# Kernel tuning notes

Hardware: AMD Instinct MI355X
Metric: run time of the kernel (lower is better)

The kernel has to match this reference:

```python
import jax, jax.numpy as jnp
import numpy as np

R = 2            # radius
KS = 2 * R + 1   # kernel size = 5
K2 = KS * KS     # 25 neighbors per pixel
TOPK = 10
TAU = 0.1
EPS = 1e-8


def _unfold(x):
    """x: [B,C,H,W] -> patches [B,C,K2,H,W], zero-padded like F.unfold(padding=R)."""
    B, C, H, W = x.shape
    xp = jnp.pad(x, ((0, 0), (0, 0), (R, R), (R, R)))
    shifts = [xp[:, :, dy:dy + H, dx:dx + W] for dy in range(KS) for dx in range(KS)]
    return jnp.stack(shifts, axis=2)


def setup_inputs() -> dict:
    key = jax.random.key(0)
    kx, = jax.random.split(key, 1)
    x = jax.random.normal(kx, (4, 256, 56, 56), dtype=jnp.float32)
    gamma = jnp.asarray(0.2, dtype=jnp.float32)  # nn.Parameter scalar, init lam=0.2
    return {"x": x, "gamma": gamma}


def reference(x, gamma):
    xd = jax.lax.stop_gradient(x)  # detach_target=True
    patches = _unfold(xd)                         # [B,C,K2,H,W]
    center = xd[:, :, None]                       # [B,C,1,H,W]
    # cosine similarity over channel dim, scaled by 1/tau
    dot = jnp.sum(patches * center, axis=1)       # [B,K2,H,W]
    pn = jnp.sqrt(jnp.sum(patches * patches, axis=1))
    cn = jnp.sqrt(jnp.sum(center * center, axis=1))
    sims = dot / jnp.maximum(pn * cn, EPS) / TAU  # [B,K2,H,W]
    # top-k mask along neighbor dim, then softmax over kept entries
    s = jnp.moveaxis(sims, 1, -1)                 # [B,H,W,K2]
    _, idx = jax.lax.top_k(s, TOPK)               # idx: [B,H,W,TOPK]
    keep = jnp.sum(jax.nn.one_hot(idx, K2, dtype=jnp.float32), axis=-2) > 0  # [B,H,W,K2]
    masked = jnp.where(keep, s, -jnp.inf)
    w = jax.nn.softmax(masked, axis=-1)           # [B,H,W,K2]
    w = jnp.moveaxis(w, -1, 1)                    # [B,K2,H,W]
    y = jnp.einsum('bckhw,bkhw->bchw', patches, w)
    return x + gamma * y
```

## Files before the change

kernel.cpp:

```cpp
#include <hip/hip_runtime.h>
#include <hip/hip_bf16.h>


#define PX 3136
#define CS 3136

typedef float f4a __attribute__((ext_vector_type(4), aligned(4)));

#define DECODE_SLAB()                                   \
    const int bid   = blockIdx.x;                       \
    const int xcd   = bid & 7;                          \
    const int b     = xcd >> 1;                         \
    const int pbase = (((xcd & 1) * 49) + (bid >> 3)) * 32;

__global__ __launch_bounds__(1024) void k_dot(const float* __restrict__ x,
                                              float* __restrict__ dot) {
    DECODE_SLAB();
    const int px = threadIdx.x & 31;
    const int ck = threadIdx.x >> 5;
    const int p  = pbase + px;
    const int h  = p / 56;
    const int w  = p - h * 56;

    const bool vm2 = (h >= 2), vm1 = (h >= 1);
    const bool cv0 = (w >= 2), cv1 = (w >= 1), cv3 = (w <= 54), cv4 = (w <= 53);

    const float* xb  = x + (size_t)b * 256 * CS + (size_t)ck * 8 * CS;
    const float* cp  = xb + p;
    const float* pr2 = cp - 112;
    const float* pr1 = cp - 56;

    float a[13];
    #pragma unroll
    for (int i = 0; i < 13; ++i) a[i] = 0.f;

    {
        const float ctr = cp[0];
        float n;
        n = (vm2 && cv0) ? pr2[-2] : 0.f; a[0]  = fmaf(ctr, n, a[0]);
        n = (vm2 && cv1) ? pr2[-1] : 0.f; a[1]  = fmaf(ctr, n, a[1]);
        n =  vm2         ? pr2[ 0] : 0.f; a[2]  = fmaf(ctr, n, a[2]);
        n = (vm2 && cv3) ? pr2[ 1] : 0.f; a[3]  = fmaf(ctr, n, a[3]);
        n = (vm2 && cv4) ? pr2[ 2] : 0.f; a[4]  = fmaf(ctr, n, a[4]);
        n = (vm1 && cv0) ? pr1[-2] : 0.f; a[5]  = fmaf(ctr, n, a[5]);
        n = (vm1 && cv1) ? pr1[-1] : 0.f; a[6]  = fmaf(ctr, n, a[6]);
        n =  vm1         ? pr1[ 0] : 0.f; a[7]  = fmaf(ctr, n, a[7]);
        n = (vm1 && cv3) ? pr1[ 1] : 0.f; a[8]  = fmaf(ctr, n, a[8]);
        n = (vm1 && cv4) ? pr1[ 2] : 0.f; a[9]  = fmaf(ctr, n, a[9]);
        n =  cv0         ? cp [-2] : 0.f; a[10] = fmaf(ctr, n, a[10]);
        n =  cv1         ? cp [-1] : 0.f; a[11] = fmaf(ctr, n, a[11]);
        a[12] = fmaf(ctr, ctr, a[12]);
    }

    const bool tail_unsafe = (b == 3) && (ck == 31);

    #pragma unroll
    for (int c = 1; c < 8; ++c) {
        const int o = c * CS;
        if (c == 7 && tail_unsafe) {
            const f4a   t2  = *(const f4a*)(pr2 + o - 2);
            const float t2e = pr2[o + 2];
            const f4a   t1  = *(const f4a*)(pr1 + o - 2);
            const float t1e = pr1[o + 2];
            const float c0  = cp[o - 2], c1 = cp[o - 1], ctr = cp[o];
            a[0]  = fmaf(ctr, t2.x, a[0]);
            a[1]  = fmaf(ctr, t2.y, a[1]);
            a[2]  = fmaf(ctr, t2.z, a[2]);
            a[3]  = fmaf(ctr, t2.w, a[3]);
            a[4]  = fmaf(ctr, t2e,  a[4]);
            a[5]  = fmaf(ctr, t1.x, a[5]);
            a[6]  = fmaf(ctr, t1.y, a[6]);
            a[7]  = fmaf(ctr, t1.z, a[7]);
            a[8]  = fmaf(ctr, t1.w, a[8]);
            a[9]  = fmaf(ctr, t1e,  a[9]);
            a[10] = fmaf(ctr, c0,   a[10]);
            a[11] = fmaf(ctr, c1,   a[11]);
            a[12] = fmaf(ctr, ctr,  a[12]);
        } else {
            const f4a   t2  = *(const f4a*)(pr2 + o - 2);
            const float t2e = pr2[o + 2];
            const f4a   t1  = *(const f4a*)(pr1 + o - 2);
            const float t1e = pr1[o + 2];
            const f4a   t0  = *(const f4a*)(cp  + o - 2);
            const float ctr = t0.z;
            a[0]  = fmaf(ctr, t2.x, a[0]);
            a[1]  = fmaf(ctr, t2.y, a[1]);
            a[2]  = fmaf(ctr, t2.z, a[2]);
            a[3]  = fmaf(ctr, t2.w, a[3]);
            a[4]  = fmaf(ctr, t2e,  a[4]);
            a[5]  = fmaf(ctr, t1.x, a[5]);
            a[6]  = fmaf(ctr, t1.y, a[6]);
            a[7]  = fmaf(ctr, t1.z, a[7]);
            a[8]  = fmaf(ctr, t1.w, a[8]);
            a[9]  = fmaf(ctr, t1e,  a[9]);
            a[10] = fmaf(ctr, t0.x, a[10]);
            a[11] = fmaf(ctr, t0.y, a[11]);
            a[12] = fmaf(ctr, ctr,  a[12]);
        }
    }

    __shared__ float part[32][13][32];
    #pragma unroll
    for (int i = 0; i < 13; ++i) part[ck][i][px] = a[i];
    __syncthreads();

    if (threadIdx.x < 13 * 32) {
        const int acc = threadIdx.x >> 5, pp = threadIdx.x & 31;
        float s = 0.f;
        #pragma unroll
        for (int j = 0; j < 32; ++j) s += part[j][acc][pp];
        dot[((size_t)(b * 13 + acc)) * PX + pbase + pp] = s;
    }
}

__global__ __launch_bounds__(1024) void k_fused(const float* __restrict__ x,
                                                const float* __restrict__ dot,
                                                const float* __restrict__ gptr,
                                                float* __restrict__ out) {
    DECODE_SLAB();
    const int tid = threadIdx.x;
    const float* db = dot + (size_t)b * 13 * PX;

    __shared__ float s_lds[32][25];
    __shared__ float e_lds[32][25];
    __shared__ float inv_lds[32];

    if (tid < 800) {
        const int px = tid / 25, k = tid - (tid / 25) * 25;
        const int p = pbase + px;
        const int h = p / 56, w = p - (p / 56) * 56;
        const int dy = k / 5 - 2, dx = k % 5 - 2;
        const int rr = h + dy, cc = w + dx;
        const bool v = (rr >= 0) && (rr < 56) && (cc >= 0) && (cc < 56);
        float d = 0.f, n2 = 0.f;
        if (v) {
            const int q = rr * 56 + cc;
            n2 = db[12 * PX + q];
            d  = (k <= 12) ? db[k * PX + p] : db[(24 - k) * PX + q];
        }
        const float cn = sqrtf(db[12 * PX + p]);
        s_lds[px][k] = d / fmaxf(sqrtf(n2) * cn, 1e-8f) * 10.f;
    }
    __syncthreads();

    if (tid < 800) {
        const int px = tid / 25, k = tid - (tid / 25) * 25;
        const float sk = s_lds[px][k];
        int rank = 0;
        float m = sk;
        #pragma unroll
        for (int j = 0; j < 25; ++j) {
            const float sj = s_lds[px][j];
            rank += (int)((sj > sk) || ((sj == sk) && (j < k)));
            m = fmaxf(m, sj);
        }
        e_lds[px][k] = (rank < 10) ? __expf(sk - m) : 0.f;
    }
    __syncthreads();

    if (tid < 32) {
        float denom = 0.f;
        #pragma unroll
        for (int k = 0; k < 25; ++k) denom += e_lds[tid][k];
        inv_lds[tid] = 1.f / denom;
    }
    __syncthreads();

    const int px  = tid & 31;
    const int sub = tid >> 5;
    const int p   = pbase + px;
    const int h   = p / 56;
    const int w   = p - h * 56;
    const float g = *gptr;

    const bool vm2 = (h >= 2), vm1 = (h >= 1), vp1 = (h <= 54), vp2 = (h <= 53);
    const bool cv0 = (w >= 2), cv1 = (w >= 1), cv3 = (w <= 54), cv4 = (w <= 53);

    const float inv = inv_lds[px];
    float wq[25];
    #pragma unroll
    for (int k = 0; k < 25; ++k) {
        const int dy = k / 5 - 2, dx = k % 5 - 2;
        const bool vr = (dy == -2) ? vm2 : (dy == -1) ? vm1 : (dy == 0) ? true
                      : (dy == 1) ? vp1 : vp2;
        const bool vc = (dx == -2) ? cv0 : (dx == -1) ? cv1 : (dx == 0) ? true
                      : (dx == 1) ? cv3 : cv4;
        wq[k] = (vr && vc) ? e_lds[px][k] * inv : 0.f;
    }

    const float* xb = x   + ((size_t)b * 256 + sub * 8) * CS;
    float*       ob = out + ((size_t)b * 256 + sub * 8) * CS;

    #pragma unroll 2
    for (int ci = 0; ci < 8; ++ci) {
        const float* xp = xb + ci * CS + p;
        const bool unsafe = (b == 0 && sub == 0 && ci == 0) ||
                            (b == 3 && sub == 31 && ci == 7);
        float y = 0.f, ctr;
        if (!unsafe) {
            #pragma unroll
            for (int r = 0; r < 5; ++r) {
                const float* rp = xp + (r - 2) * 56;
                const f4a   v4 = *(const f4a*)(rp - 2);
                const float s4 = rp[2];
                if (r == 2) ctr = v4.z;
                y = fmaf(wq[r*5+0], v4.x, y);
                y = fmaf(wq[r*5+1], v4.y, y);
                y = fmaf(wq[r*5+2], v4.z, y);
                y = fmaf(wq[r*5+3], v4.w, y);
                y = fmaf(wq[r*5+4], s4,   y);
            }
        } else {
            ctr = xp[0];
            #pragma unroll
            for (int k = 0; k < 25; ++k) {
                const int dy = k / 5 - 2, dx = k % 5 - 2;
                const bool vr = (dy == -2) ? vm2 : (dy == -1) ? vm1 : (dy == 0) ? true
                              : (dy == 1) ? vp1 : vp2;
                const bool vc = (dx == -2) ? cv0 : (dx == -1) ? cv1 : (dx == 0) ? true
                              : (dx == 1) ? cv3 : cv4;
                const float xv = (vr && vc) ? xp[dy * 56 + dx] : 0.f;
                y = fmaf(wq[k], xv, y);
            }
        }
        ob[ci * CS + p] = ctr + g * y;
    }
}

extern "C" void kernel_launch(void* const* d_in, const int* in_sizes, int n_in,
                              void* d_out, int out_size, void* d_ws, size_t ws_size,
                              hipStream_t stream) {
    const float* x     = (const float*)d_in[0];
    const float* gamma = (const float*)d_in[1];
    float* out = (float*)d_out;
    float* dot = (float*)d_ws;

    k_dot<<<392, 1024, 0, stream>>>(x, dot);
    k_fused<<<392, 1024, 0, stream>>>(x, dot, gamma, out);
}
```

Measured before the change: 32.53 us.

## Map k_fused blocks to image rows and share neighbors via wave shuffles

The fused kernel now gives each block one full image row (56 pixels, 224 blocks) instead of 32-pixel slabs. Each lane of a 64-wide wave owns one column and loads five row values per channel. Horizontal neighbors come from cross-lane shuffles instead of overlapping unaligned vector loads, and edge handling uses clamped row offsets plus zeroed weights. This drops the special 'unsafe' path and the redundant loads, but leaves 8 of 64 lanes idle, runs fewer blocks, and gives each wave 16 channels.

After: 36.57 us. +12.4%, slower.

```diff
diff --git a/kernel.cpp b/kernel.cpp
--- a/kernel.cpp
+++ b/kernel.cpp
@@ -117,20 +117,22 @@
                                                 const float* __restrict__ dot,
                                                 const float* __restrict__ gptr,
                                                 float* __restrict__ out) {
-    DECODE_SLAB();
+    const int bid = blockIdx.x;
+    const int xcd = bid & 7;
+    const int b   = xcd >> 1;
+    const int h   = (xcd & 1) * 28 + (bid >> 3);
     const int tid = threadIdx.x;
     const float* db = dot + (size_t)b * 13 * PX;
 
-    __shared__ float s_lds[32][25];
-    __shared__ float e_lds[32][25];
-    __shared__ float inv_lds[32];
-
-    if (tid < 800) {
-        const int px = tid / 25, k = tid - (tid / 25) * 25;
-        const int p = pbase + px;
-        const int h = p / 56, w = p - (p / 56) * 56;
+    __shared__ float s_lds[56][25];
+    __shared__ float e_lds[56][25];
+    __shared__ float inv_lds[56];
+
+    for (int i = tid; i < 1400; i += 1024) {
+        const int px = i / 25, k = i - px * 25;
+        const int p = h * 56 + px;
         const int dy = k / 5 - 2, dx = k % 5 - 2;
-        const int rr = h + dy, cc = w + dx;
+        const int rr = h + dy, cc = px + dx;
         const bool v = (rr >= 0) && (rr < 56) && (cc >= 0) && (cc < 56);
         float d = 0.f, n2 = 0.f;
         if (v) {
@@ -143,8 +145,8 @@
     }
     __syncthreads();
 
-    if (tid < 800) {
-        const int px = tid / 25, k = tid - (tid / 25) * 25;
+    for (int i = tid; i < 1400; i += 1024) {
+        const int px = i / 25, k = i - px * 25;
         const float sk = s_lds[px][k];
         int rank = 0;
         float m = sk;
@@ -158,7 +160,7 @@
     }
     __syncthreads();
 
-    if (tid < 32) {
+    if (tid < 56) {
         float denom = 0.f;
         #pragma unroll
         for (int k = 0; k < 25; ++k) denom += e_lds[tid][k];
@@ -166,65 +168,55 @@
     }
     __syncthreads();
 
-    const int px  = tid & 31;
-    const int sub = tid >> 5;
-    const int p   = pbase + px;
-    const int h   = p / 56;
-    const int w   = p - h * 56;
-    const float g = *gptr;
-
-    const bool vm2 = (h >= 2), vm1 = (h >= 1), vp1 = (h <= 54), vp2 = (h <= 53);
-    const bool cv0 = (w >= 2), cv1 = (w >= 1), cv3 = (w <= 54), cv4 = (w <= 53);
-
-    const float inv = inv_lds[px];
+    const int lane = tid & 63;
+    const int wave = tid >> 6;
+    const int wc   = (lane < 56) ? lane : 55;
+    const float g  = *gptr;
+
+    const float inv = inv_lds[wc];
     float wq[25];
     #pragma unroll
     for (int k = 0; k < 25; ++k) {
         const int dy = k / 5 - 2, dx = k % 5 - 2;
-        const bool vr = (dy == -2) ? vm2 : (dy == -1) ? vm1 : (dy == 0) ? true
-                      : (dy == 1) ? vp1 : vp2;
-        const bool vc = (dx == -2) ? cv0 : (dx == -1) ? cv1 : (dx == 0) ? true
-                      : (dx == 1) ? cv3 : cv4;
-        wq[k] = (vr && vc) ? e_lds[px][k] * inv : 0.f;
-    }
-
-    const float* xb = x   + ((size_t)b * 256 + sub * 8) * CS;
-    float*       ob = out + ((size_t)b * 256 + sub * 8) * CS;
+        const int rr = h + dy, cc = lane + dx;
+        const bool v = (rr >= 0) && (rr < 56) && (cc >= 0) && (cc < 56) &&
+                       (lane < 56);
+        wq[k] = v ? e_lds[wc][k] * inv : 0.f;
+    }
+
+    const int rm2 = ((h >= 2) ? h - 2 : 0) * 56;
+    const int rm1 = ((h >= 1) ? h - 1 : 0) * 56;
+    const int r0  = h * 56;
+    const int rp1 = ((h <= 54) ? h + 1 : 55) * 56;
+    const int rp2 = ((h <= 53) ? h + 2 : 55) * 56;
+
+    const float* xb = x   + ((size_t)b * 256 + wave * 16) * CS;
+    float*       ob = out + ((size_t)b * 256 + wave * 16) * CS;
+
+#define ROW5(vr, base)                                         \
+    y = fmaf(wq[(base)+0], __shfl((vr), lane - 2, 64), y);     \
+    y = fmaf(wq[(base)+1], __shfl((vr), lane - 1, 64), y);     \
+    y = fmaf(wq[(base)+2], (vr), y);                           \
+    y = fmaf(wq[(base)+3], __shfl((vr), lane + 1, 64), y);     \
+    y = fmaf(wq[(base)+4], __shfl((vr), lane + 2, 64), y);
 
     #pragma unroll 2
-    for (int ci = 0; ci < 8; ++ci) {
-        const float* xp = xb + ci * CS + p;
-        const bool unsafe = (b == 0 && sub == 0 && ci == 0) ||
-                            (b == 3 && sub == 31 && ci == 7);
-        float y = 0.f, ctr;
-        if (!unsafe) {
-            #pragma unroll
-            for (int r = 0; r < 5; ++r) {
-                const float* rp = xp + (r - 2) * 56;
-                const f4a   v4 = *(const f4a*)(rp - 2);
-                const float s4 = rp[2];
-                if (r == 2) ctr = v4.z;
-                y = fmaf(wq[r*5+0], v4.x, y);
-                y = fmaf(wq[r*5+1], v4.y, y);
-                y = fmaf(wq[r*5+2], v4.z, y);
-                y = fmaf(wq[r*5+3], v4.w, y);
-                y = fmaf(wq[r*5+4], s4,   y);
-            }
-        } else {
-            ctr = xp[0];
-            #pragma unroll
-            for (int k = 0; k < 25; ++k) {
-                const int dy = k / 5 - 2, dx = k % 5 - 2;
-                const bool vr = (dy == -2) ? vm2 : (dy == -1) ? vm1 : (dy == 0) ? true
-                              : (dy == 1) ? vp1 : vp2;
-                const bool vc = (dx == -2) ? cv0 : (dx == -1) ? cv1 : (dx == 0) ? true
-                              : (dx == 1) ? cv3 : cv4;
-                const float xv = (vr && vc) ? xp[dy * 56 + dx] : 0.f;
-                y = fmaf(wq[k], xv, y);
-            }
-        }
-        ob[ci * CS + p] = ctr + g * y;
-    }
+    for (int ci = 0; ci < 16; ++ci) {
+        const float* xc = xb + ci * CS;
+        const float v0 = xc[rm2 + wc];
+        const float v1 = xc[rm1 + wc];
+        const float v2 = xc[r0  + wc];
+        const float v3 = xc[rp1 + wc];
+        const float v4 = xc[rp2 + wc];
+        float y = 0.f;
+        ROW5(v0, 0)
+        ROW5(v1, 5)
+        ROW5(v2, 10)
+        ROW5(v3, 15)
+        ROW5(v4, 20)
+        if (lane < 56) ob[ci * CS + r0 + lane] = v2 + g * y;
+    }
+#undef ROW5
 }
 
 extern "C" void kernel_launch(void* const* d_in, const int* in_sizes, int n_in,
@@ -236,5 +228,5 @@
     float* dot = (float*)d_ws;
 
     k_dot<<<392, 1024, 0, stream>>>(x, dot);
-    k_fused<<<392, 1024, 0, stream>>>(x, dot, gamma, out);
+    k_fused<<<224, 1024, 0, stream>>>(x, dot, gamma, out);
 }
```

## Stage input row tiles in LDS for the weighted neighbor aggregation

Applied to the files above, without the earlier changes.

The aggregation phase no longer reads 5x5 neighborhoods straight from global memory. It now loops over 8 groups of 32 channels, cooperatively copying the six needed image rows per channel into shared memory (clamped at the image borders), and computes the weighted sum from LDS. Each thread now owns one channel per group instead of eight consecutive channels. The aim is to drop redundant global and L1 neighborhood loads and the special-case path for unsafe boundary reads. In exchange it adds two block-wide barriers per group, serializes the load and compute phases, and uses about 43KB of LDS. Column-boundary taps can read uninitialized padding words, which are only cancelled by zero weights.

Measured after the change: 38.46 us. 1.18x slower.

```diff
diff --git a/kernel.cpp b/kernel.cpp
--- a/kernel.cpp
+++ b/kernel.cpp
@@ -121,6 +121,7 @@
     const int tid = threadIdx.x;
     const float* db = dot + (size_t)b * 13 * PX;
 
+    __shared__ float dlds[32 * 336 + 8];
     __shared__ float s_lds[32][25];
     __shared__ float e_lds[32][25];
     __shared__ float inv_lds[32];
@@ -173,6 +174,10 @@
     const int w   = p - h * 56;
     const float g = *gptr;
 
+    const int r0    = pbase / 56;
+    const int rbase = r0 - 2;
+    const int lrow  = h - rbase;
+
     const bool vm2 = (h >= 2), vm1 = (h >= 1), vp1 = (h <= 54), vp2 = (h <= 53);
     const bool cv0 = (w >= 2), cv1 = (w >= 1), cv3 = (w <= 54), cv4 = (w <= 53);
 
@@ -188,42 +193,42 @@
         wq[k] = (vr && vc) ? e_lds[px][k] * inv : 0.f;
     }
 
-    const float* xb = x   + ((size_t)b * 256 + sub * 8) * CS;
-    float*       ob = out + ((size_t)b * 256 + sub * 8) * CS;
-
-    #pragma unroll 2
-    for (int ci = 0; ci < 8; ++ci) {
-        const float* xp = xb + ci * CS + p;
-        const bool unsafe = (b == 0 && sub == 0 && ci == 0) ||
-                            (b == 3 && sub == 31 && ci == 7);
-        float y = 0.f, ctr;
-        if (!unsafe) {
-            #pragma unroll
-            for (int r = 0; r < 5; ++r) {
-                const float* rp = xp + (r - 2) * 56;
-                const f4a   v4 = *(const f4a*)(rp - 2);
-                const float s4 = rp[2];
-                if (r == 2) ctr = v4.z;
-                y = fmaf(wq[r*5+0], v4.x, y);
-                y = fmaf(wq[r*5+1], v4.y, y);
-                y = fmaf(wq[r*5+2], v4.z, y);
-                y = fmaf(wq[r*5+3], v4.w, y);
-                y = fmaf(wq[r*5+4], s4,   y);
-            }
-        } else {
-            ctr = xp[0];
-            #pragma unroll
-            for (int k = 0; k < 25; ++k) {
-                const int dy = k / 5 - 2, dx = k % 5 - 2;
-                const bool vr = (dy == -2) ? vm2 : (dy == -1) ? vm1 : (dy == 0) ? true
-                              : (dy == 1) ? vp1 : vp2;
-                const bool vc = (dx == -2) ? cv0 : (dx == -1) ? cv1 : (dx == 0) ? true
-                              : (dx == 1) ? cv3 : cv4;
-                const float xv = (vr && vc) ? xp[dy * 56 + dx] : 0.f;
-                y = fmaf(wq[k], xv, y);
-            }
-        }
-        ob[ci * CS + p] = ctr + g * y;
+    int srow[6];
+    #pragma unroll
+    for (int j = 0; j < 6; ++j) {
+        int r = rbase + j;
+        srow[j] = (r < 0) ? 0 : ((r > 55) ? 55 : r);
+    }
+
+    const float* xb = x   + (size_t)b * 256 * CS;
+    float*       ob = out + (size_t)b * 256 * CS;
+    const int cbl = 4 + sub * 336 + lrow * 56 + w;
+
+    for (int grp = 0; grp < 8; ++grp) {
+        __syncthreads();
+        for (int j = tid; j < 2688; j += 1024) {
+            const int ch  = j / 84;
+            const int rem = j - ch * 84;
+            const int rj  = rem / 14;
+            const int q4  = rem - rj * 14;
+            const float* src = xb + ((size_t)(grp * 32 + ch)) * CS
+                             + srow[rj] * 56 + q4 * 4;
+            *(f4a*)(dlds + 4 + ch * 336 + rj * 56 + q4 * 4) = *(const f4a*)src;
+        }
+        __syncthreads();
+
+        float y = 0.f;
+        #pragma unroll
+        for (int r = 0; r < 5; ++r) {
+            const int base = cbl + (r - 2) * 56;
+            y = fmaf(wq[r*5+0], dlds[base - 2], y);
+            y = fmaf(wq[r*5+1], dlds[base - 1], y);
+            y = fmaf(wq[r*5+2], dlds[base    ], y);
+            y = fmaf(wq[r*5+3], dlds[base + 1], y);
+            y = fmaf(wq[r*5+4], dlds[base + 2], y);
+        }
+        const float ctr = dlds[cbl];
+        ob[((size_t)(grp * 32 + sub)) * CS + p] = ctr + g * y;
     }
 }
 
```
